# Optimization experiments

Measured on AMD Instinct MI355X. Metric: run time of the kernel, lower is better.

## Reference

```python
import jax, jax.numpy as jnp
import numpy as np

B, C, S, H, W = 1, 256, 64, 32, 128
BLOCKS, HEADS, DH = 2, 8, 32
SCALE = DH ** (-0.5)


def layer_norm(x, w, b, eps=1e-5):
    mu = jnp.mean(x, axis=-1, keepdims=True)
    var = jnp.var(x, axis=-1, keepdims=True)
    return (x - mu) * jax.lax.rsqrt(var + eps) * w + b


def generate_y_for_attn(y, u):
    # y: (B,C,H,W), u: (B,S,S) float -> (B, S^2, 2H, C)
    Bv, Cv, Hv, Wv = y.shape
    Sv = u.shape[1]
    uf = jnp.floor(u).reshape(Bv, Sv * Sv)
    u_left = jnp.clip(uf, 0, Wv - 1).astype(jnp.int32)
    u_right = jnp.clip(uf + 1, 0, Wv - 1).astype(jnp.int32)
    yf = y.reshape(Bv, Cv * Hv, Wv)

    def gather_w(idx):
        idxb = jnp.broadcast_to(idx[:, None, :], (Bv, Cv * Hv, Sv * Sv))
        return jnp.take_along_axis(yf, idxb, axis=2).reshape(Bv, Cv, Hv, Sv * Sv)

    ys = jnp.concatenate([gather_w(u_left), gather_w(u_right)], axis=2)  # (B,C,2H,S2)
    return ys.transpose(0, 3, 2, 1)  # (B, S2, 2H, C)


def cross_attention(x, y, p, i):
    # x: (B,M,C), y: (B,M,N,C)
    q = layer_norm(x, p['ln_q_w'][i], p['ln_q_b'][i]) @ p['Wq'][i]        # (B,M,HD)
    k = layer_norm(y, p['ln_k_w'][i], p['ln_k_b'][i]) @ p['Wk'][i]        # (B,M,N,HD)
    v = layer_norm(y, p['ln_v_w'][i], p['ln_v_b'][i]) @ p['Wv'][i]        # (B,M,N,HD)
    Bv, M, _ = q.shape
    N = k.shape[2]
    q = q.reshape(Bv, M, HEADS, DH)
    k = k.reshape(Bv, M, N, HEADS, DH)
    v = v.reshape(Bv, M, N, HEADS, DH)
    dot = SCALE * jnp.einsum('bmhd,bmnhd->bhmn', q, k)                    # (B,H,M,N)
    attn = jax.nn.softmax(dot, axis=-1)
    a = jnp.einsum('bhmn,bmnhd->bmhd', attn, v).reshape(Bv, M, HEADS * DH)
    z = a @ p['Wproj'][i] + p['bproj'][i]
    z = layer_norm(z, p['ln_pre_w'][i], p['ln_pre_b'][i])
    h = jax.nn.gelu(z @ p['Wm1'][i] + p['bm1'][i], approximate=False)
    z = z + (h @ p['Wm2'][i] + p['bm2'][i])
    return layer_norm(z, p['ln_post_w'][i], p['ln_post_b'][i])


def setup_inputs() -> dict:
    key = jax.random.key(0)
    ks = jax.random.split(key, 16)
    std = 0.02
    inp = {
        'grd2sat': jax.random.normal(ks[0], (B, C, S, S), jnp.float32),
        'grd_x': jax.random.normal(ks[1], (B, C, H, W), jnp.float32),
        'u': jax.random.uniform(ks[2], (B, S, S), jnp.float32) * (W - 1),
        'ln_q_w': jnp.ones((BLOCKS, C)), 'ln_q_b': jnp.zeros((BLOCKS, C)),
        'ln_k_w': jnp.ones((BLOCKS, C)), 'ln_k_b': jnp.zeros((BLOCKS, C)),
        'ln_v_w': jnp.ones((BLOCKS, C)), 'ln_v_b': jnp.zeros((BLOCKS, C)),
        'Wq': std * jax.random.normal(ks[3], (BLOCKS, C, HEADS * DH)),
        'Wk': std * jax.random.normal(ks[4], (BLOCKS, C, HEADS * DH)),
        'Wv': std * jax.random.normal(ks[5], (BLOCKS, C, HEADS * DH)),
        'Wproj': std * jax.random.normal(ks[6], (BLOCKS, HEADS * DH, C)),
        'bproj': jnp.zeros((BLOCKS, C)),
        'ln_pre_w': jnp.ones((BLOCKS, C)), 'ln_pre_b': jnp.zeros((BLOCKS, C)),
        'Wm1': std * jax.random.normal(ks[7], (BLOCKS, C, 2 * C)),
        'bm1': jnp.zeros((BLOCKS, 2 * C)),
        'Wm2': std * jax.random.normal(ks[8], (BLOCKS, 2 * C, C)),
        'bm2': jnp.zeros((BLOCKS, C)),
        'ln_post_w': jnp.ones((BLOCKS, C)), 'ln_post_b': jnp.zeros((BLOCKS, C)),
    }
    return inp


def reference(grd2sat, grd_x, u, ln_q_w, ln_q_b, ln_k_w, ln_k_b, ln_v_w, ln_v_b,
              Wq, Wk, Wv, Wproj, bproj, ln_pre_w, ln_pre_b, Wm1, bm1, Wm2, bm2,
              ln_post_w, ln_post_b):
    p = dict(ln_q_w=ln_q_w, ln_q_b=ln_q_b, ln_k_w=ln_k_w, ln_k_b=ln_k_b,
             ln_v_w=ln_v_w, ln_v_b=ln_v_b, Wq=Wq, Wk=Wk, Wv=Wv, Wproj=Wproj,
             bproj=bproj, ln_pre_w=ln_pre_w, ln_pre_b=ln_pre_b, Wm1=Wm1, bm1=bm1,
             Wm2=Wm2, bm2=bm2, ln_post_w=ln_post_w, ln_post_b=ln_post_b)
    y_attn = generate_y_for_attn(grd_x, u)               # (B, S^2, 2H, C)
    x = grd2sat.reshape(B, C, S * S).transpose(0, 2, 1)  # (B, M, C)
    for i in range(BLOCKS):
        # (Swin self-attention layer omitted; cross-attention stack only.)
        x = cross_attention(x, y_attn, p, i)
    out = x.transpose(0, 2, 1).reshape(B, C, S, S)
    # L2 normalize over channel dim
    norm = jnp.sqrt(jnp.sum(out * out, axis=1, keepdims=True))
    return out / jnp.maximum(norm, 1e-12)
```

## Files before the change

### kernel.cpp

```cpp
#include <hip/hip_runtime.h>
#include <math.h>


#define C_DIM 256
#define M_DIM 4096
#define W_DIM 128
#define H_DIM 32
#define ATT_SCALE 0.17677669529663687f

typedef __attribute__((ext_vector_type(8))) short short8;
typedef __attribute__((ext_vector_type(4))) short short4v;
typedef __attribute__((ext_vector_type(4))) float floatx4;

__device__ __forceinline__ unsigned short f2bf(float f) {
    unsigned u = __float_as_uint(f);
    unsigned r = (u + 0x7fffu + ((u >> 16) & 1u)) >> 16;
    return (unsigned short)r;
}
__device__ __forceinline__ float gelu_exact(float x) {
    return 0.5f * x * (1.0f + erff(x * 0.70710678118654752f));
}

struct PrepArgs {
    const float* grd2sat; float* xcur;
// ... 11 lines not shown
    int b = blockIdx.x, t = threadIdx.x;
    if (b < 256) {
        float (*tile)[65] = (float(*)[65])smemf;
        int m0 = (b & 63) << 6, c0 = (b >> 6) << 6;
        for (int it = 0; it < 16; ++it) {
            int idx = it * 256 + t;
            int co = idx >> 6, mo = idx & 63;
            tile[co][mo] = a.grd2sat[(size_t)(c0 + co) * M_DIM + m0 + mo];
        }
        __syncthreads();
        for (int it = 0; it < 16; ++it) {
            int idx = it * 256 + t;
            int mo = idx >> 6, co = idx & 63;
            a.xcur[(size_t)(m0 + mo) * C_DIM + c0 + co] = tile[co][mo];
        }
    } else if (b < 384) {
        int idx = b - 256;
        int h = idx & 31, w0 = (idx >> 5) << 5;
        float (*tile)[33] = (float(*)[33])smemf;
        float (*ps)[32] = (float(*)[32])(smemf + 8448);
        float (*pss)[32] = (float(*)[32])(smemf + 8704);
        float* mu_s = smemf + 8960;
        float* rs_s = smemf + 8992;
        int wo = t & 31, cb = t >> 5;
        for (int it = 0; it < 32; ++it) {
            int c = it * 8 + cb;
            tile[c][wo] = a.grd_x[(size_t)c * (H_DIM * W_DIM) + h * W_DIM + w0 + wo];
        }
        __syncthreads();
        {
            int w = t & 31, part = t >> 5;
            float s = 0.f, ss = 0.f;
            for (int c = part * 32; c < part * 32 + 32; ++c) {
                float x = tile[c][w];
                s += x; ss += x * x;
            }
            ps[part][w] = s; pss[part][w] = ss;
        }
        __syncthreads();
        if (t < 32) {
            float s = 0.f, ss = 0.f;
            for (int p = 0; p < 8; ++p) { s += ps[p][t]; ss += pss[p][t]; }
            float mu = s * (1.f / 256.f);
            float var = ss * (1.f / 256.f) - mu * mu;
            mu_s[t] = mu;
            rs_s[t] = rsqrtf(var + 1e-5f);
        }
        __syncthreads();
        for (int jj = 0; jj < 32; ++jj) {
            float mu = mu_s[jj], rs = rs_s[jj];
            a.yhat[((size_t)(w0 + jj) * H_DIM + h) * C_DIM + t] =
                (tile[t][jj] - mu) * rs;
        }
    } else if (b < 1408) {
        int wI = b - 384;
        int e = 0;
        while (wI >= a.wbase[e + 1]) ++e;
        int tl = wI - a.wbase[e];
        int tilesC = a.wC[e] >> 5;
        int tr = tl / tilesC, tc = tl - tr * tilesC;
        int r0 = tr << 5, c0 = tc << 5;
        const float* in = a.win[e];
        unsigned short* out = a.wout[e];
        const float* lnw = a.wlnw[e];
        int R = a.wR[e], Cc = a.wC[e];
        float (*tile)[33] = (float(*)[33])smemf;
        int rl = t >> 3, cq = (t & 7) << 2;
        float4 v = *(const float4*)&in[(size_t)(r0 + rl) * Cc + c0 + cq];
        if (lnw) {
            float s = lnw[r0 + rl];
            v.x *= s; v.y *= s; v.z *= s; v.w *= s;
        }
        tile[rl][cq + 0] = v.x;
        tile[rl][cq + 1] = v.y;
        tile[rl][cq + 2] = v.z;
        tile[rl][cq + 3] = v.w;
        __syncthreads();
        int cl = t >> 3, rq = (t & 7) << 2;
        ushort4 o;
        o.x = f2bf(tile[rq + 0][cl]);
        o.y = f2bf(tile[rq + 1][cl]);
        o.z = f2bf(tile[rq + 2][cl]);
        o.w = f2bf(tile[rq + 3][cl]);
        *(ushort4*)&out[(size_t)(c0 + cl) * R + r0 + rq] = o;
    } else if (b < 1418) {
        int jj = b - 1408;
        int N = a.fN[jj];
        int wcol = a.fwcol[jj] + t;
        const float* W = a.fW[jj];
        const float* lb = a.flnb[jj];
        float s = a.fbase[jj] ? a.fbase[jj][wcol] : 0.f;
        for (int k = 0; k < 256; ++k) s += lb[k] * W[(size_t)k * N + wcol];
        a.fout[jj][a.focol[jj] + t] = s;
    } else {
        int* hist = (int*)smemf;
        int* cur = (int*)smemf + 128;
        unsigned short* wlb = (unsigned short*)((int*)smemf + 256);
        if (t < 128) hist[t] = 0;
        __syncthreads();
        for (int it = 0; it < 16; ++it) {
            int m = it * 256 + t;
            int wl = (int)floorf(a.u[m]);
            wl = max(0, min(wl, 126));
            wlb[m] = (unsigned short)wl;
            atomicAdd(&hist[wl], 1);
        }
        __syncthreads();
        if (t == 0) {
            int run = 0, nc = 0;
            for (int bkt = 0; bkt < 127; ++bkt) {
                int c = hist[bkt];
                cur[bkt] = run;
                int q0 = run;
                while (c > 0) {
                    int take = min(c, 32);
                    a.chunks[nc] = make_int4(bkt, q0, take, 0);
                    ++nc; q0 += take; c -= take;
                }
                run += hist[bkt];
            }
            *a.nchunks = nc;
        }
        __syncthreads();
        for (int it = 0; it < 16; ++it) {
            int m = it * 256 + t;
            int wl = wlb[m];
            int pos = atomicAdd(&cur[wl], 1);
            a.perm[pos] = m;
        }
    }
}

struct GJ {
    const void* A; const unsigned short* Bt;
    const float* bias; const float* aw; const float* ab;
    const float* rw; const float* rb; const float* res;
    float* wrz; void* out; unsigned short* out2;
    int K, N;
};

template <int LN, int EPI, int OUTM, bool WRZ, bool ABF16>
__device__ __forceinline__ void gemm_core(const GJ& j, short (*As)[264],
                                          short (*Bs)[264], int bm, int by) {
    int t = threadIdx.x;
    int bn = by << 6;
    int wv = t >> 6, lane = t & 63;
    int mt = wv & 1, nt0 = (wv >> 1) << 1;
    int quad = lane >> 4, l16 = lane & 15;
    floatx4 acc0 = {0.f, 0.f, 0.f, 0.f};
    floatx4 acc1 = {0.f, 0.f, 0.f, 0.f};
    const int K = j.K;
    for (int kc = 0; kc < K; kc += 256) {
        if (kc) __syncthreads();
        if (ABF16) {
            int ar = t >> 3, cq = (t & 7) << 5;
            const unsigned short* ap =
                (const unsigned short*)j.A + (size_t)(bm + ar) * K + kc + cq;
#pragma unroll
            for (int c = 0; c < 4; ++c)
                *(uint4*)&As[ar][cq + (c << 3)] = *(const uint4*)(ap + (c << 3));
        } else {
            int ar = t >> 3, cq = (t & 7) << 2;
            const float* ap = (const float*)j.A + (size_t)(bm + ar) * K + kc + cq;
            float4 v[8];
#pragma unroll
            for (int g = 0; g < 8; ++g) v[g] = *(const float4*)(ap + g * 32);
            if (LN >= 1) {
                float s = 0.f, ss = 0.f;
#pragma unroll
                for (int g = 0; g < 8; ++g) {
                    s += v[g].x + v[g].y + v[g].z + v[g].w;
                    ss += v[g].x * v[g].x + v[g].y * v[g].y + v[g].z * v[g].z +
                          v[g].w * v[g].w;
                }
#pragma unroll
                for (int o = 1; o < 8; o <<= 1) {
                    s += __shfl_xor(s, o, 64);
                    ss += __shfl_xor(ss, o, 64);
                }
                float mu = s * (1.f / 256.f);
                float rs = rsqrtf(ss * (1.f / 256.f) - mu * mu + 1e-5f);
#pragma unroll
                for (int g = 0; g < 8; ++g) {
                    v[g].x = (v[g].x - mu) * rs;
                    v[g].y = (v[g].y - mu) * rs;
                    v[g].z = (v[g].z - mu) * rs;
                    v[g].w = (v[g].w - mu) * rs;
                }
            }
#pragma unroll
            for (int g = 0; g < 8; ++g) {
                short4v o;
                o[0] = (short)f2bf(v[g].x);
                o[1] = (short)f2bf(v[g].y);
                o[2] = (short)f2bf(v[g].z);
                o[3] = (short)f2bf(v[g].w);
                *(short4v*)&As[ar][cq + g * 32] = o;
            }
        }
        {
            int br = t >> 2, cq2 = (t & 3) << 3;
            const unsigned short* bp = j.Bt + (size_t)(bn + br) * K + kc + cq2;
#pragma unroll
            for (int g = 0; g < 8; ++g)
                *(short8*)&Bs[br][cq2 + g * 32] = *(const short8*)(bp + g * 32);
        }
        __syncthreads();
#pragma unroll
        for (int k0 = 0; k0 < 8; ++k0) {
            short8 aa = *(const short8*)&As[(mt << 4) + l16][(k0 << 5) + (quad << 3)];
            short8 b0 = *(const short8*)&Bs[(nt0 << 4) + l16][(k0 << 5) + (quad << 3)];
            short8 b1 =
                *(const short8*)&Bs[((nt0 + 1) << 4) + l16][(k0 << 5) + (quad << 3)];
            acc0 = __builtin_amdgcn_mfma_f32_16x16x32_bf16(aa, b0, acc0, 0, 0, 0);
            acc1 = __builtin_amdgcn_mfma_f32_16x16x32_bf16(aa, b1, acc1, 0, 0, 0);
        }
    }
#pragma unroll
    for (int jj = 0; jj < 2; ++jj) {
        const floatx4 accv = jj ? acc1 : acc0;
        int col = bn + ((nt0 + jj) << 4) + l16;
        float bv = j.bias ? j.bias[col] : 0.f;
#pragma unroll
        for (int r = 0; r < 4; ++r) {
            int row = bm + (mt << 4) + (quad << 2) + r;
            float v = accv[r] + bv;
            if (OUTM == 0) {
                ((float*)j.out)[(size_t)row * j.N + col] = v;
            } else if (OUTM == 1) {
                ((unsigned short*)j.out)[(size_t)row * j.N + col] = f2bf(v);
            } else {
                if (col < 256)
                    ((unsigned short*)j.out)[(size_t)row * 256 + col] = f2bf(v);
                else
                    j.out2[(size_t)(col - 256) * M_DIM + row] = f2bf(v);
            }
        }
    }
}

__global__ __launch_bounds__(256) void kv_kernel(GJ j0, GJ j1) {
    __shared__ short As[32][264];
    __shared__ short Bs[64][264];
    int bm = blockIdx.x << 5;
    if ((int)blockIdx.y < 8)
        gemm_core<0, 0, 2, false, false>(j0, As, Bs, bm, blockIdx.y);
    else
        gemm_core<0, 0, 2, false, false>(j1, As, Bs, bm, blockIdx.y - 8);
}

struct MegaArgs {
    const float* xcur;
    const int* perm; const int4* chunks; const int* nchunks;
    float* xfinal;
    const unsigned short* Wq[2]; const unsigned short* Wp[2];
    const unsigned short* Wm1[2]; const unsigned short* Wm2[2];
    const unsigned short* Ktb[2]; const unsigned short* Vtb[2];
    const float* qb[2]; const float* m1b[2];
    const float* bpj[2]; const float* bm2v[2];
    const float* pw[2]; const float* pb[2];
    const float* aw; const float* ab;
};

__device__ __forceinline__ void cg_pass(const short* As, int lda,
                                        const unsigned short* Bt, int K, int bn,
                                        short (*Bst)[264], floatx4& acc0,
                                        floatx4& acc1) {
    int t = threadIdx.x;
    int wv = t >> 6, lane = t & 63, quad = lane >> 4, l16 = lane & 15;
    int mt = wv & 1, nt0 = (wv >> 1) << 1;
    int br = t >> 2, cq2 = (t & 3) << 3;
#pragma unroll 1
    for (int kc = 0; kc < K; kc += 256) {
        const unsigned short* bp = Bt + (size_t)(bn + br) * K + kc + cq2;
#pragma unroll
        for (int g = 0; g < 8; ++g)
            *(short8*)&Bst[br][cq2 + (g << 5)] = *(const short8*)(bp + (g << 5));
        __syncthreads();
        const short* ap = As + (size_t)((mt << 4) + l16) * lda + kc + (quad << 3);
#pragma unroll
        for (int k0 = 0; k0 < 8; ++k0) {
            short8 aa = *(const short8*)(ap + (k0 << 5));
            short8 b0 =
                *(const short8*)&Bst[(nt0 << 4) + l16][(k0 << 5) + (quad << 3)];
            short8 b1 =
                *(const short8*)&Bst[((nt0 + 1) << 4) + l16][(k0 << 5) + (quad << 3)];
            acc0 = __builtin_amdgcn_mfma_f32_16x16x32_bf16(aa, b0, acc0, 0, 0, 0);
            acc1 = __builtin_amdgcn_mfma_f32_16x16x32_bf16(aa, b1, acc1, 0, 0, 0);
        }
        __syncthreads();
    }
}

__global__ __launch_bounds__(256) void mega_kernel(MegaArgs a) {
    __shared__ __align__(16) char smem[150656];
    short (*XH)[264] = (short(*)[264])(smem);
    short (*HH)[520] = (short(*)[520])(smem);
    short (*QR)[264] = (short(*)[264])(smem + 33280);
    float (*Zf)[260] = (float(*)[260])(smem + 33280);
    short (*ZH)[264] = (short(*)[264])(smem + 66560);
    short (*AR)[264] = (short(*)[264])(smem + 83456);
    float (*XO)[260] = (float(*)[260])(smem + 83456);
    short (*Bst)[264] = (short(*)[264])(smem + 116736);
    float (*SS)[69] = (float(*)[69])(smem + 116736);
    short (*PB)[72] = (short(*)[72])(smem + 116736 + 8832);
    int* gp = (int*)(smem + 150528);

    if ((int)blockIdx.x >= *a.nchunks) return;
    int4 cd = a.chunks[blockIdx.x];
    int wl = cd.x, qstart = cd.y, qcnt = cd.z;
    int t = threadIdx.x;
    if (t < 32) gp[t] = (t < qcnt) ? a.perm[qstart + t] : a.perm[qstart];
    __syncthreads();

    int wv = t >> 6, lane = t & 63, quad = lane >> 4, l16 = lane & 15;
    int mt = wv & 1, nt0 = (wv >> 1) << 1, ntP = wv >> 1;
    int r8 = t >> 3, cq = (t & 7) << 5;
    int sg = t & 7;

#pragma unroll 1
    for (int l = 0; l < 2; ++l) {
        {
            float4 v[8];
            if (l == 0) {
                const float* xp = a.xcur + (size_t)gp[r8] * 256 + cq;
#pragma unroll
                for (int g = 0; g < 8; ++g) v[g] = *(const float4*)(xp + (g << 2));
            } else {
#pragma unroll
                for (int g = 0; g < 8; ++g)
                    v[g] = *(const float4*)&XO[r8][cq + (g << 2)];
            }
            float s = 0.f, ss = 0.f;
#pragma unroll
            for (int g = 0; g < 8; ++g) {
                s += v[g].x + v[g].y + v[g].z + v[g].w;
                ss += v[g].x * v[g].x + v[g].y * v[g].y + v[g].z * v[g].z +
                      v[g].w * v[g].w;
            }
#pragma unroll
            for (int o = 1; o < 8; o <<= 1) {
                s += __shfl_xor(s, o, 64);
                ss += __shfl_xor(ss, o, 64);
            }
            float mu = s * (1.f / 256.f);
            float rs = rsqrtf(ss * (1.f / 256.f) - mu * mu + 1e-5f);
#pragma unroll
            for (int g = 0; g < 8; ++g) {
                v[g].x = (v[g].x - mu) * rs;
                v[g].y = (v[g].y - mu) * rs;
                v[g].z = (v[g].z - mu) * rs;
                v[g].w = (v[g].w - mu) * rs;
            }
            if (l == 1) {
                float s2 = 0.f, ss2 = 0.f;
#pragma unroll
                for (int g = 0; g < 8; ++g) {
                    float4 w4 = *(const float4*)&a.aw[cq + (g << 2)];
                    float4 b4 = *(const float4*)&a.ab[cq + (g << 2)];
                    v[g].x = v[g].x * w4.x + b4.x;
                    v[g].y = v[g].y * w4.y + b4.y;
                    v[g].z = v[g].z * w4.z + b4.z;
                    v[g].w = v[g].w * w4.w + b4.w;
                    s2 += v[g].x + v[g].y + v[g].z + v[g].w;
                    ss2 += v[g].x * v[g].x + v[g].y * v[g].y + v[g].z * v[g].z +
                           v[g].w * v[g].w;
                }
#pragma unroll
                for (int o = 1; o < 8; o <<= 1) {
                    s2 += __shfl_xor(s2, o, 64);
                    ss2 += __shfl_xor(ss2, o, 64);
                }
                float mu2 = s2 * (1.f / 256.f);
                float rs2 = rsqrtf(ss2 * (1.f / 256.f) - mu2 * mu2 + 1e-5f);
#pragma unroll
                for (int g = 0; g < 8; ++g) {
                    v[g].x = (v[g].x - mu2) * rs2;
                    v[g].y = (v[g].y - mu2) * rs2;
                    v[g].z = (v[g].z - mu2) * rs2;
                    v[g].w = (v[g].w - mu2) * rs2;
                }
            }
#pragma unroll
            for (int g = 0; g < 8; ++g) {
                short4v o;
                o[0] = (short)f2bf(v[g].x);
                o[1] = (short)f2bf(v[g].y);
                o[2] = (short)f2bf(v[g].z);
                o[3] = (short)f2bf(v[g].w);
                *(short4v*)&XH[r8][cq + (g << 2)] = o;
            }
        }
        __syncthreads();

        {
            const float* qb = a.qb[l];
#pragma unroll 1
            for (int bn = 0; bn < 256; bn += 64) {
                floatx4 a0 = {0.f, 0.f, 0.f, 0.f};
                floatx4 a1 = {0.f, 0.f, 0.f, 0.f};
                cg_pass((const short*)XH, 264, a.Wq[l], 256, bn, Bst, a0, a1);
#pragma unroll
                for (int jj = 0; jj < 2; ++jj) {
                    const floatx4 av = jj ? a1 : a0;
                    int col = bn + ((nt0 + jj) << 4) + l16;
                    float bv = qb[col];
#pragma unroll
                    for (int r = 0; r < 4; ++r)
                        QR[(mt << 4) + (quad << 2) + r][col] =
                            (short)f2bf(av[r] + bv);
                }
            }
        }
        __syncthreads();

        {
            const unsigned short* kp0 =
                a.Ktb[l] + ((size_t)((wl << 5) + (nt0 << 4) + l16)) * 256;
            const unsigned short* kp1 = kp0 + (16 * 256);
            const unsigned short* vpb =
                a.Vtb[l] + (size_t)((ntP << 4) + l16) * M_DIM + (wl << 5);
            short8 qa = *(const short8*)&QR[(mt << 4) + l16][(quad << 3)];
            short8 kb0 = *(const short8*)(kp0 + (quad << 3));
            short8 kb1 = *(const short8*)(kp1 + (quad << 3));
            short8 va0 = *(const short8*)(vpb + (quad << 3));
            short8 va1 = *(const short8*)(vpb + 32 + (quad << 3));
#pragma unroll 1
            for (int h = 0; h < 8; ++h) {
                {
                    floatx4 zz = {0.f, 0.f, 0.f, 0.f};
                    floatx4 c0 =
                        __builtin_amdgcn_mfma_f32_16x16x32_bf16(qa, kb0, zz, 0, 0, 0);
                    floatx4 c1 =
                        __builtin_amdgcn_mfma_f32_16x16x32_bf16(qa, kb1, zz, 0, 0, 0);
#pragma unroll
                    for (int r = 0; r < 4; ++r) {
                        int row = (mt << 4) + (quad << 2) + r;
                        SS[row][(nt0 << 4) + l16] = c0[r];
                        SS[row][((nt0 + 1) << 4) + l16] = c1[r];
                    }
                }
                short8 nva0 = va0, nva1 = va1;
                if (h < 7) {
                    int hn = h + 1;
                    qa = *(const short8*)&QR[(mt << 4) + l16][(hn << 5) + (quad << 3)];
                    kb0 = *(const short8*)(kp0 + (hn << 5) + (quad << 3));
                    kb1 = *(const short8*)(kp1 + (hn << 5) + (quad << 3));
                    const unsigned short* vpn = vpb + (size_t)(hn << 5) * M_DIM;
                    nva0 = *(const short8*)(vpn + (quad << 3));
                    nva1 = *(const short8*)(vpn + 32 + (quad << 3));
                }
                __syncthreads();
                {
                    float e[8];
                    float s = 0.f;
#pragma unroll
                    for (int c = 0; c < 8; ++c) {
                        e[c] = __expf(SS[r8][(sg << 3) + c] * ATT_SCALE);
                        s += e[c];
                    }
                    s += __shfl_xor(s, 1, 64);
                    s += __shfl_xor(s, 2, 64);
                    s += __shfl_xor(s, 4, 64);
                    float ri = 1.f / s;
#pragma unroll
                    for (int c = 0; c < 8; ++c)
                        PB[r8][(sg << 3) + c] = (short)f2bf(e[c] * ri);
                }
                __syncthreads();
                {
                    floatx4 acc = {0.f, 0.f, 0.f, 0.f};
#pragma unroll
                    for (int ks = 0; ks < 2; ++ks) {
                        short8 pa = *(const short8*)&PB[(mt << 4) + l16]
                                                      [(ks << 5) + (quad << 3)];
                        short8 vb = ks ? va1 : va0;
                        acc = __builtin_amdgcn_mfma_f32_16x16x32_bf16(pa, vb, acc,
                                                                      0, 0, 0);
                    }
#pragma unroll
                    for (int r = 0; r < 4; ++r)
                        AR[(mt << 4) + (quad << 2) + r]
                          [(h << 5) + (ntP << 4) + l16] = (short)f2bf(acc[r]);
                }
                va0 = nva0;
                va1 = nva1;
            }
        }
        __syncthreads();

        {
            const float* bpj = a.bpj[l];
#pragma unroll 1
            for (int bn = 0; bn < 256; bn += 64) {
                floatx4 a0 = {0.f, 0.f, 0.f, 0.f};
                floatx4 a1 = {0.f, 0.f, 0.f, 0.f};
                cg_pass((const short*)AR, 264, a.Wp[l], 256, bn, Bst, a0, a1);
#pragma unroll
                for (int jj = 0; jj < 2; ++jj) {
                    const floatx4 av = jj ? a1 : a0;
                    int col = bn + ((nt0 + jj) << 4) + l16;
                    float bv = bpj[col];
#pragma unroll
                    for (int r = 0; r < 4; ++r)
                        Zf[(mt << 4) + (quad << 2) + r][col] = av[r] + bv;
                }
            }
        }
        __syncthreads();

        {
            const float* pw = a.pw[l];
            const float* pb = a.pb[l];
            float4 v[8];
#pragma unroll
            for (int g = 0; g < 8; ++g) v[g] = *(const float4*)&Zf[r8][cq + (g << 2)];
            float s = 0.f, ss = 0.f;
#pragma unroll
            for (int g = 0; g < 8; ++g) {
                s += v[g].x + v[g].y + v[g].z + v[g].w;
                ss += v[g].x * v[g].x + v[g].y * v[g].y + v[g].z * v[g].z +
                      v[g].w * v[g].w;
            }
#pragma unroll
            for (int o = 1; o < 8; o <<= 1) {
                s += __shfl_xor(s, o, 64);
                ss += __shfl_xor(ss, o, 64);
            }
            float mu = s * (1.f / 256.f);
            float rs = rsqrtf(ss * (1.f / 256.f) - mu * mu + 1e-5f);
#pragma unroll
            for (int g = 0; g < 8; ++g) {
                float4 z;
                z.x = (v[g].x - mu) * rs;
                z.y = (v[g].y - mu) * rs;
                z.z = (v[g].z - mu) * rs;
                z.w = (v[g].w - mu) * rs;
                short4v o;
                o[0] = (short)f2bf(z.x);
                o[1] = (short)f2bf(z.y);
                o[2] = (short)f2bf(z.z);
                o[3] = (short)f2bf(z.w);
                *(short4v*)&ZH[r8][cq + (g << 2)] = o;
                float4 w4 = *(const float4*)&pw[cq + (g << 2)];
                float4 b4 = *(const float4*)&pb[cq + (g << 2)];
                float4 za;
                za.x = z.x * w4.x + b4.x;
                za.y = z.y * w4.y + b4.y;
                za.z = z.z * w4.z + b4.z;
                za.w = z.w * w4.w + b4.w;
                *(float4*)&Zf[r8][cq + (g << 2)] = za;
            }
        }
        __syncthreads();

        {
            const float* m1b = a.m1b[l];
#pragma unroll 1
            for (int bn = 0; bn < 512; bn += 64) {
                floatx4 a0 = {0.f, 0.f, 0.f, 0.f};
                floatx4 a1 = {0.f, 0.f, 0.f, 0.f};
                cg_pass((const short*)ZH, 264, a.Wm1[l], 256, bn, Bst, a0, a1);
#pragma unroll
                for (int jj = 0; jj < 2; ++jj) {
                    const floatx4 av = jj ? a1 : a0;
                    int col = bn + ((nt0 + jj) << 4) + l16;
                    float bv = m1b[col];
#pragma unroll
                    for (int r = 0; r < 4; ++r)
                        HH[(mt << 4) + (quad << 2) + r][col] =
                            (short)f2bf(gelu_exact(av[r] + bv));
                }
            }
        }
        __syncthreads();

        {
            const float* b2 = a.bm2v[l];
#pragma unroll 1
            for (int bn = 0; bn < 256; bn += 64) {
                floatx4 a0 = {0.f, 0.f, 0.f, 0.f};
                floatx4 a1 = {0.f, 0.f, 0.f, 0.f};
                cg_pass((const short*)HH, 520, a.Wm2[l], 512, bn, Bst, a0, a1);
#pragma unroll
                for (int jj = 0; jj < 2; ++jj) {
                    const floatx4 av = jj ? a1 : a0;
                    int col = bn + ((nt0 + jj) << 4) + l16;
                    float bv = b2[col];
#pragma unroll
                    for (int r = 0; r < 4; ++r) {
                        int row = (mt << 4) + (quad << 2) + r;
                        float v = av[r] + bv + Zf[row][col];
                        if (l == 0) {
                            XO[row][col] = v;
                        } else if (row < qcnt) {
                            a.xfinal[(size_t)gp[row] * 256 + col] = v;
                        }
                    }
                }
            }
        }
        __syncthreads();
    }
}

__global__ __launch_bounds__(256) void out_kernel(const float* __restrict__ X,
                                                  const float* __restrict__ w,
                                                  const float* __restrict__ b,
                                                  float* __restrict__ out) {
    __shared__ float tile[64][65];
    int t = threadIdx.x;
    int mo = t >> 2, q = t & 3;
    int m0 = blockIdx.x << 6;
    const float* p = X + (size_t)(m0 + mo) * C_DIM + (q << 6);
    float4 v[16];
    float s = 0.f, ss = 0.f;
#pragma unroll
    for (int c = 0; c < 16; ++c) {
        v[c] = *(const float4*)(p + c * 4);
        s += v[c].x + v[c].y + v[c].z + v[c].w;
        ss += v[c].x * v[c].x + v[c].y * v[c].y + v[c].z * v[c].z + v[c].w * v[c].w;
    }
    s += __shfl_xor(s, 1, 64); s += __shfl_xor(s, 2, 64);
    ss += __shfl_xor(ss, 1, 64); ss += __shfl_xor(ss, 2, 64);
    float mu = s * (1.f / 256.f);
    float rs = rsqrtf(ss * (1.f / 256.f) - mu * mu + 1e-5f);
    float ss2 = 0.f;
#pragma unroll
    for (int c = 0; c < 16; ++c) {
        float4 w4 = *(const float4*)&w[(q << 6) + c * 4];
        float4 b4 = *(const float4*)&b[(q << 6) + c * 4];
        v[c].x = (v[c].x - mu) * rs * w4.x + b4.x;
        v[c].y = (v[c].y - mu) * rs * w4.y + b4.y;
        v[c].z = (v[c].z - mu) * rs * w4.z + b4.z;
        v[c].w = (v[c].w - mu) * rs * w4.w + b4.w;
        ss2 += v[c].x * v[c].x + v[c].y * v[c].y + v[c].z * v[c].z + v[c].w * v[c].w;
    }
    ss2 += __shfl_xor(ss2, 1, 64); ss2 += __shfl_xor(ss2, 2, 64);
    float sc = 1.f / fmaxf(sqrtf(ss2), 1e-12f);
    for (int cc = 0; cc < 4; ++cc) {
        if (q == cc) {
#pragma unroll
            for (int c = 0; c < 16; ++c) {
                tile[mo][c * 4 + 0] = v[c].x * sc;
                tile[mo][c * 4 + 1] = v[c].y * sc;
                tile[mo][c * 4 + 2] = v[c].z * sc;
                tile[mo][c * 4 + 3] = v[c].w * sc;
            }
        }
        __syncthreads();
        for (int it = 0; it < 16; ++it) {
            int idx = it * 256 + t;
            int co = idx >> 6, mr = idx & 63;
            out[(size_t)((cc << 6) + co) * M_DIM + m0 + mr] = tile[mr][co];
        }
        __syncthreads();
    }
}

extern "C" void kernel_launch(void* const* d_in, const int* in_sizes, int n_in,
                              void* d_out, int out_size, void* d_ws, size_t ws_size,
                              hipStream_t stream) {
    const float* grd2sat = (const float*)d_in[0];
    const float* grd_x   = (const float*)d_in[1];
    const float* u       = (const float*)d_in[2];
    const float* ln_q_w  = (const float*)d_in[3];
    const float* ln_q_b  = (const float*)d_in[4];
    const float* ln_k_w  = (const float*)d_in[5];
    const float* ln_k_b  = (const float*)d_in[6];
    const float* ln_v_w  = (const float*)d_in[7];
    const float* ln_v_b  = (const float*)d_in[8];
    const float* Wq      = (const float*)d_in[9];
    const float* Wk      = (const float*)d_in[10];
    const float* Wv      = (const float*)d_in[11];
    const float* Wproj   = (const float*)d_in[12];
    const float* bproj   = (const float*)d_in[13];
    const float* ln_pre_w = (const float*)d_in[14];
    const float* ln_pre_b = (const float*)d_in[15];
    const float* Wm1     = (const float*)d_in[16];
    const float* bm1     = (const float*)d_in[17];
    const float* Wm2     = (const float*)d_in[18];
    const float* bm2     = (const float*)d_in[19];
    const float* ln_post_w = (const float*)d_in[20];
    const float* ln_post_b = (const float*)d_in[21];

    float* ws   = (float*)d_ws;
    float* yhat = ws;
    float* xcur = ws + 1048576;
    float* zq   = ws + 2097152;
    unsigned short* Ktab0 = (unsigned short*)(ws + 6291456);
    unsigned short* Vt0   = (unsigned short*)(ws + 6815744);
    unsigned short* Ktab1 = (unsigned short*)(ws + 7340032);
    unsigned short* Vt1   = (unsigned short*)(ws + 7864320);
    unsigned short* Bt    = (unsigned short*)(ws + 8388608);
    float* biasbuf = ws + 8912896;
    int*  perm    = (int*)(ws + 8915456);
    int4* chunks  = (int4*)(ws + 8919552);
    int*  nchunks = (int*)(ws + 8921600);
    const size_t BS = 524288;
    const size_t OQ = 0, OKV = 65536, OP = 196608, OM1 = 262144, OM2 = 393216;

    dim3 b256(256);

    PrepArgs pa;
    pa.grd2sat = grd2sat; pa.xcur = xcur;
    pa.grd_x = grd_x;     pa.yhat = yhat;
    pa.u = u; pa.perm = perm; pa.chunks = chunks; pa.nchunks = nchunks;
    {
        int base = 0;
        for (int i = 0; i < 2; ++i) {
            int e = 6 * i;
            unsigned short* bt = Bt + i * BS;
            pa.win[e+0] = Wq + i * 65536;    pa.wout[e+0] = bt + OQ;
            pa.wlnw[e+0] = ln_q_w + i * 256; pa.wR[e+0] = 256; pa.wC[e+0] = 256;
            pa.win[e+1] = Wk + i * 65536;    pa.wout[e+1] = bt + OKV;
            pa.wlnw[e+1] = ln_k_w + i * 256; pa.wR[e+1] = 256; pa.wC[e+1] = 256;
            pa.win[e+2] = Wv + i * 65536;    pa.wout[e+2] = bt + OKV + 65536;
            pa.wlnw[e+2] = ln_v_w + i * 256; pa.wR[e+2] = 256; pa.wC[e+2] = 256;
            pa.win[e+3] = Wproj + i * 65536; pa.wout[e+3] = bt + OP;
            pa.wlnw[e+3] = nullptr;          pa.wR[e+3] = 256; pa.wC[e+3] = 256;
            pa.win[e+4] = Wm1 + i * 131072;  pa.wout[e+4] = bt + OM1;
            pa.wlnw[e+4] = ln_pre_w + i * 256; pa.wR[e+4] = 256; pa.wC[e+4] = 512;
            pa.win[e+5] = Wm2 + i * 131072;  pa.wout[e+5] = bt + OM2;
            pa.wlnw[e+5] = nullptr;          pa.wR[e+5] = 512; pa.wC[e+5] = 256;
        }
        for (int e = 0; e < 12; ++e) {
            pa.wbase[e] = base;
            base += (pa.wR[e] >> 5) * (pa.wC[e] >> 5);
        }
        pa.wbase[12] = base;
        for (int i = 0; i < 2; ++i) {
            int jb = 5 * i;
            float* bb = biasbuf + i * 1280;
            pa.fW[jb+0] = Wq + i * 65536; pa.flnb[jb+0] = ln_q_b + i * 256;
            pa.fbase[jb+0] = nullptr; pa.fout[jb+0] = bb;
            pa.fN[jb+0] = 256; pa.fwcol[jb+0] = 0; pa.focol[jb+0] = 0;
            pa.fW[jb+1] = Wk + i * 65536; pa.flnb[jb+1] = ln_k_b + i * 256;
            pa.fbase[jb+1] = nullptr; pa.fout[jb+1] = bb + 256;
            pa.fN[jb+1] = 256; pa.fwcol[jb+1] = 0; pa.focol[jb+1] = 0;
            pa.fW[jb+2] = Wv + i * 65536; pa.flnb[jb+2] = ln_v_b + i * 256;
            pa.fbase[jb+2] = nullptr; pa.fout[jb+2] = bb + 256;
            pa.fN[jb+2] = 256; pa.fwcol[jb+2] = 0; pa.focol[jb+2] = 256;
            pa.fW[jb+3] = Wm1 + i * 131072; pa.flnb[jb+3] = ln_pre_b + i * 256;
            pa.fbase[jb+3] = bm1 + i * 512; pa.fout[jb+3] = bb + 768;
            pa.fN[jb+3] = 512; pa.fwcol[jb+3] = 0; pa.focol[jb+3] = 0;
            pa.fW[jb+4] = Wm1 + i * 131072; pa.flnb[jb+4] = ln_pre_b + i * 256;
            pa.fbase[jb+4] = bm1 + i * 512; pa.fout[jb+4] = bb + 768;
            pa.fN[jb+4] = 512; pa.fwcol[jb+4] = 256; pa.focol[jb+4] = 256;
        }
    }
// ... 32 lines not shown
```

Before: 238.4 us.

## Read weights directly from global in mega kernel GEMMs with 8-tile register accumulators

Replaces the LDS-staged B-tile GEMM passes (cg_pass, with two syncs per 64-column chunk) with mgemm8, which loads weight fragments straight from global/L2 into registers and has each wave accumulate 8 output tiles (128 columns). The attention stage is restructured to process heads in pairs, with separate score, softmax and PV phases and per-pair score/probability buffers. The MLP is split into two 256-wide halves so the hidden buffer fits in reused LDS. Shared memory drops and launch bounds are set to one block, trading LDS staging and barriers for more global load traffic and higher register pressure. Unused template branches in the KV GEMM are also removed.

```diff
diff --git a/kernel.cpp b/kernel.cpp
--- a/kernel.cpp
+++ b/kernel.cpp
@@ -187,42 +187,12 @@
     const int K = j.K;
     for (int kc = 0; kc < K; kc += 256) {
         if (kc) __syncthreads();
-        if (ABF16) {
-            int ar = t >> 3, cq = (t & 7) << 5;
-            const unsigned short* ap =
-                (const unsigned short*)j.A + (size_t)(bm + ar) * K + kc + cq;
-#pragma unroll
-            for (int c = 0; c < 4; ++c)
-                *(uint4*)&As[ar][cq + (c << 3)] = *(const uint4*)(ap + (c << 3));
-        } else {
+        {
             int ar = t >> 3, cq = (t & 7) << 2;
             const float* ap = (const float*)j.A + (size_t)(bm + ar) * K + kc + cq;
             float4 v[8];
 #pragma unroll
             for (int g = 0; g < 8; ++g) v[g] = *(const float4*)(ap + g * 32);
-            if (LN >= 1) {
-                float s = 0.f, ss = 0.f;
-#pragma unroll
-                for (int g = 0; g < 8; ++g) {
-                    s += v[g].x + v[g].y + v[g].z + v[g].w;
-                    ss += v[g].x * v[g].x + v[g].y * v[g].y + v[g].z * v[g].z +
-                          v[g].w * v[g].w;
-                }
-#pragma unroll
-                for (int o = 1; o < 8; o <<= 1) {
-                    s += __shfl_xor(s, o, 64);
-                    ss += __shfl_xor(ss, o, 64);
-                }
-                float mu = s * (1.f / 256.f);
-                float rs = rsqrtf(ss * (1.f / 256.f) - mu * mu + 1e-5f);
-#pragma unroll
-                for (int g = 0; g < 8; ++g) {
-                    v[g].x = (v[g].x - mu) * rs;
-                    v[g].y = (v[g].y - mu) * rs;
-                    v[g].z = (v[g].z - mu) * rs;
-                    v[g].w = (v[g].w - mu) * rs;
-                }
-            }
 #pragma unroll
             for (int g = 0; g < 8; ++g) {
                 short4v o;
@@ -260,16 +230,10 @@
         for (int r = 0; r < 4; ++r) {
             int row = bm + (mt << 4) + (quad << 2) + r;
             float v = accv[r] + bv;
-            if (OUTM == 0) {
-                ((float*)j.out)[(size_t)row * j.N + col] = v;
-            } else if (OUTM == 1) {
-                ((unsigned short*)j.out)[(size_t)row * j.N + col] = f2bf(v);
-            } else {
-                if (col < 256)
-                    ((unsigned short*)j.out)[(size_t)row * 256 + col] = f2bf(v);
-                else
-                    j.out2[(size_t)(col - 256) * M_DIM + row] = f2bf(v);
-            }
+            if (col < 256)
+                ((unsigned short*)j.out)[(size_t)row * 256 + col] = f2bf(v);
+            else
+                j.out2[(size_t)(col - 256) * M_DIM + row] = f2bf(v);
         }
     }
 }
@@ -297,49 +261,35 @@
     const float* aw; const float* ab;
 };
 
-__device__ __forceinline__ void cg_pass(const short* As, int lda,
-                                        const unsigned short* Bt, int K, int bn,
-                                        short (*Bst)[264], floatx4& acc0,
-                                        floatx4& acc1) {
-    int t = threadIdx.x;
-    int wv = t >> 6, lane = t & 63, quad = lane >> 4, l16 = lane & 15;
-    int mt = wv & 1, nt0 = (wv >> 1) << 1;
-    int br = t >> 2, cq2 = (t & 3) << 3;
-#pragma unroll 1
-    for (int kc = 0; kc < K; kc += 256) {
-        const unsigned short* bp = Bt + (size_t)(bn + br) * K + kc + cq2;
-#pragma unroll
-        for (int g = 0; g < 8; ++g)
-            *(short8*)&Bst[br][cq2 + (g << 5)] = *(const short8*)(bp + (g << 5));
-        __syncthreads();
-        const short* ap = As + (size_t)((mt << 4) + l16) * lda + kc + (quad << 3);
-#pragma unroll
-        for (int k0 = 0; k0 < 8; ++k0) {
-            short8 aa = *(const short8*)(ap + (k0 << 5));
-            short8 b0 =
-                *(const short8*)&Bst[(nt0 << 4) + l16][(k0 << 5) + (quad << 3)];
-            short8 b1 =
-                *(const short8*)&Bst[((nt0 + 1) << 4) + l16][(k0 << 5) + (quad << 3)];
-            acc0 = __builtin_amdgcn_mfma_f32_16x16x32_bf16(aa, b0, acc0, 0, 0, 0);
-            acc1 = __builtin_amdgcn_mfma_f32_16x16x32_bf16(aa, b1, acc1, 0, 0, 0);
-        }
-        __syncthreads();
-    }
-}
-
-__global__ __launch_bounds__(256) void mega_kernel(MegaArgs a) {
-    __shared__ __align__(16) char smem[150656];
+__device__ __forceinline__ void mgemm8(const short* As, int lda,
+                                       const unsigned short* Bt, int Kstride,
+                                       int kcB, int laneRow, int colbase,
+                                       int quad, int l16, floatx4 acc[8]) {
+    const short* ap = As + (size_t)laneRow * lda + (quad << 3);
+    const unsigned short* bp =
+        Bt + (size_t)(colbase + l16) * Kstride + kcB + (quad << 3);
+#pragma unroll
+    for (int k0 = 0; k0 < 8; ++k0) {
+        short8 aa = *(const short8*)(ap + (k0 << 5));
+#pragma unroll
+        for (int i = 0; i < 8; ++i) {
+            short8 bb =
+                *(const short8*)(bp + (size_t)(i << 4) * Kstride + (k0 << 5));
+            acc[i] = __builtin_amdgcn_mfma_f32_16x16x32_bf16(aa, bb, acc[i], 0, 0, 0);
+        }
+    }
+}
+
+__global__ __launch_bounds__(256, 1) void mega_kernel(MegaArgs a) {
+    __shared__ __align__(16) char smem[127616];
     short (*XH)[264] = (short(*)[264])(smem);
-    short (*HH)[520] = (short(*)[520])(smem);
-    short (*QR)[264] = (short(*)[264])(smem + 33280);
-    float (*Zf)[260] = (float(*)[260])(smem + 33280);
-    short (*ZH)[264] = (short(*)[264])(smem + 66560);
-    short (*AR)[264] = (short(*)[264])(smem + 83456);
-    float (*XO)[260] = (float(*)[260])(smem + 83456);
-    short (*Bst)[264] = (short(*)[264])(smem + 116736);
-    float (*SS)[69] = (float(*)[69])(smem + 116736);
-    short (*PB)[72] = (short(*)[72])(smem + 116736 + 8832);
-    int* gp = (int*)(smem + 150528);
+    short (*QR)[264] = (short(*)[264])(smem + 16896);
+    short (*ZH)[264] = (short(*)[264])(smem + 33792);
+    short (*AR)[264] = (short(*)[264])(smem + 50688);
+    float (*Zf)[260] = (float(*)[260])(smem + 67584);
+    float (*SS)[32][68] = (float(*)[32][68])(smem + 100864);
+    short (*PB)[32][72] = (short(*)[32][72])(smem + 118272);
+    int* gp = (int*)(smem + 127488);
 
     if ((int)blockIdx.x >= *a.nchunks) return;
     int4 cd = a.chunks[blockIdx.x];
@@ -349,29 +299,30 @@
     __syncthreads();
 
     int wv = t >> 6, lane = t & 63, quad = lane >> 4, l16 = lane & 15;
-    int mt = wv & 1, nt0 = (wv >> 1) << 1, ntP = wv >> 1;
+    int mt = wv & 1, g = wv >> 1;
+    int laneRow = (mt << 4) + l16;
+    int colbase = g << 7;
     int r8 = t >> 3, cq = (t & 7) << 5;
-    int sg = t & 7;
-
-#pragma unroll 1
+
+#pragma unroll
     for (int l = 0; l < 2; ++l) {
         {
             float4 v[8];
             if (l == 0) {
                 const float* xp = a.xcur + (size_t)gp[r8] * 256 + cq;
 #pragma unroll
-                for (int g = 0; g < 8; ++g) v[g] = *(const float4*)(xp + (g << 2));
+                for (int gg = 0; gg < 8; ++gg) v[gg] = *(const float4*)(xp + (gg << 2));
             } else {
 #pragma unroll
-                for (int g = 0; g < 8; ++g)
-                    v[g] = *(const float4*)&XO[r8][cq + (g << 2)];
+                for (int gg = 0; gg < 8; ++gg)
+                    v[gg] = *(const float4*)&Zf[r8][cq + (gg << 2)];
             }
             float s = 0.f, ss = 0.f;
 #pragma unroll
-            for (int g = 0; g < 8; ++g) {
-                s += v[g].x + v[g].y + v[g].z + v[g].w;
-                ss += v[g].x * v[g].x + v[g].y * v[g].y + v[g].z * v[g].z +
-                      v[g].w * v[g].w;
+            for (int gg = 0; gg < 8; ++gg) {
+                s += v[gg].x + v[gg].y + v[gg].z + v[gg].w;
+                ss += v[gg].x * v[gg].x + v[gg].y * v[gg].y + v[gg].z * v[gg].z +
+                      v[gg].w * v[gg].w;
             }
 #pragma unroll
             for (int o = 1; o < 8; o <<= 1) {
@@ -381,25 +332,25 @@
             float mu = s * (1.f / 256.f);
             float rs = rsqrtf(ss * (1.f / 256.f) - mu * mu + 1e-5f);
 #pragma unroll
-            for (int g = 0; g < 8; ++g) {
-                v[g].x = (v[g].x - mu) * rs;
-                v[g].y = (v[g].y - mu) * rs;
-                v[g].z = (v[g].z - mu) * rs;
-                v[g].w = (v[g].w - mu) * rs;
+            for (int gg = 0; gg < 8; ++gg) {
+                v[gg].x = (v[gg].x - mu) * rs;
+                v[gg].y = (v[gg].y - mu) * rs;
+                v[gg].z = (v[gg].z - mu) * rs;
+                v[gg].w = (v[gg].w - mu) * rs;
             }
             if (l == 1) {
                 float s2 = 0.f, ss2 = 0.f;
 #pragma unroll
-                for (int g = 0; g < 8; ++g) {
-                    float4 w4 = *(const float4*)&a.aw[cq + (g << 2)];
-                    float4 b4 = *(const float4*)&a.ab[cq + (g << 2)];
-                    v[g].x = v[g].x * w4.x + b4.x;
-                    v[g].y = v[g].y * w4.y + b4.y;
-                    v[g].z = v[g].z * w4.z + b4.z;
-                    v[g].w = v[g].w * w4.w + b4.w;
-                    s2 += v[g].x + v[g].y + v[g].z + v[g].w;
-                    ss2 += v[g].x * v[g].x + v[g].y * v[g].y + v[g].z * v[g].z +
-                           v[g].w * v[g].w;
+                for (int gg = 0; gg < 8; ++gg) {
+                    float4 w4 = *(const float4*)&a.aw[cq + (gg << 2)];
+                    float4 b4 = *(const float4*)&a.ab[cq + (gg << 2)];
+                    v[gg].x = v[gg].x * w4.x + b4.x;
+                    v[gg].y = v[gg].y * w4.y + b4.y;
+                    v[gg].z = v[gg].z * w4.z + b4.z;
+                    v[gg].w = v[gg].w * w4.w + b4.w;
+                    s2 += v[gg].x + v[gg].y + v[gg].z + v[gg].w;
+                    ss2 += v[gg].x * v[gg].x + v[gg].y * v[gg].y + v[gg].z * v[gg].z +
+                           v[gg].w * v[gg].w;
                 }
 #pragma unroll
                 for (int o = 1; o < 8; o <<= 1) {
@@ -409,137 +360,142 @@
                 float mu2 = s2 * (1.f / 256.f);
                 float rs2 = rsqrtf(ss2 * (1.f / 256.f) - mu2 * mu2 + 1e-5f);
 #pragma unroll
-                for (int g = 0; g < 8; ++g) {
-                    v[g].x = (v[g].x - mu2) * rs2;
-                    v[g].y = (v[g].y - mu2) * rs2;
-                    v[g].z = (v[g].z - mu2) * rs2;
-                    v[g].w = (v[g].w - mu2) * rs2;
-                }
-            }
-#pragma unroll
-            for (int g = 0; g < 8; ++g) {
+                for (int gg = 0; gg < 8; ++gg) {
+                    v[gg].x = (v[gg].x - mu2) * rs2;
+                    v[gg].y = (v[gg].y - mu2) * rs2;
+                    v[gg].z = (v[gg].z - mu2) * rs2;
+                    v[gg].w = (v[gg].w - mu2) * rs2;
+                }
+            }
+#pragma unroll
+            for (int gg = 0; gg < 8; ++gg) {
                 short4v o;
-                o[0] = (short)f2bf(v[g].x);
-                o[1] = (short)f2bf(v[g].y);
-                o[2] = (short)f2bf(v[g].z);
-                o[3] = (short)f2bf(v[g].w);
-                *(short4v*)&XH[r8][cq + (g << 2)] = o;
-            }
-        }
-        __syncthreads();
-
-        {
+                o[0] = (short)f2bf(v[gg].x);
+                o[1] = (short)f2bf(v[gg].y);
+                o[2] = (short)f2bf(v[gg].z);
+                o[3] = (short)f2bf(v[gg].w);
+                *(short4v*)&XH[r8][cq + (gg << 2)] = o;
+            }
+        }
+        __syncthreads();
+
+        {
+            floatx4 acc[8];
+#pragma unroll
+            for (int i = 0; i < 8; ++i) acc[i] = (floatx4){0.f, 0.f, 0.f, 0.f};
+            mgemm8((const short*)XH, 264, a.Wq[l], 256, 0, laneRow, colbase,
+                   quad, l16, acc);
             const float* qb = a.qb[l];
+#pragma unroll
+            for (int i = 0; i < 8; ++i) {
+                int col = colbase + (i << 4) + l16;
+                float bv = qb[col];
+#pragma unroll
+                for (int r = 0; r < 4; ++r)
+                    QR[(mt << 4) + (quad << 2) + r][col] = (short)f2bf(acc[i][r] + bv);
+            }
+        }
+        __syncthreads();
+
+        {
+            const unsigned short* Ktb = a.Ktb[l];
+            const unsigned short* Vtb = a.Vtb[l];
+            int p = g;
+            int mtA = mt;
+            auto scores = [&](int hd) {
+                short8 qa =
+                    *(const short8*)&QR[(mtA << 4) + l16][(hd << 5) + (quad << 3)];
+                const unsigned short* kbase =
+                    Ktb + (size_t)(wl << 5) * 256 + (hd << 5) + (quad << 3);
+                floatx4 c[4];
+#pragma unroll
+                for (int ct = 0; ct < 4; ++ct) {
+                    short8 kb =
+                        *(const short8*)(kbase + (size_t)((ct << 4) + l16) * 256);
+                    floatx4 z = {0.f, 0.f, 0.f, 0.f};
+                    c[ct] = __builtin_amdgcn_mfma_f32_16x16x32_bf16(qa, kb, z, 0, 0, 0);
+                }
+#pragma unroll
+                for (int ct = 0; ct < 4; ++ct)
+#pragma unroll
+                    for (int r = 0; r < 4; ++r)
+                        SS[p][(mtA << 4) + (quad << 2) + r][(ct << 4) + l16] =
+                            c[ct][r];
+            };
+            auto pv = [&](int hd) {
+                floatx4 o0 = {0.f, 0.f, 0.f, 0.f}, o1 = {0.f, 0.f, 0.f, 0.f};
+                const unsigned short* vb = Vtb +
+                    (size_t)((hd << 5) + l16) * M_DIM + (wl << 5) + (quad << 3);
+#pragma unroll
+                for (int ks = 0; ks < 2; ++ks) {
+                    short8 pa = *(const short8*)&PB[p][(mtA << 4) + l16]
+                                                  [(ks << 5) + (quad << 3)];
+                    short8 v0 = *(const short8*)(vb + (ks << 5));
+                    short8 v1 =
+                        *(const short8*)(vb + (size_t)16 * M_DIM + (ks << 5));
+                    o0 = __builtin_amdgcn_mfma_f32_16x16x32_bf16(pa, v0, o0, 0, 0, 0);
+                    o1 = __builtin_amdgcn_mfma_f32_16x16x32_bf16(pa, v1, o1, 0, 0, 0);
+                }
+#pragma unroll
+                for (int r = 0; r < 4; ++r) {
+                    int row = (mtA << 4) + (quad << 2) + r;
+                    AR[row][(hd << 5) + l16] = (short)f2bf(o0[r]);
+                    AR[row][(hd << 5) + 16 + l16] = (short)f2bf(o1[r]);
+                }
+            };
+            auto softmax = [&]() {
+                int p2 = t >> 7;
+                int row2 = (t >> 2) & 31;
+                int sg2 = t & 3;
+                float e[16];
+                float s = 0.f;
+#pragma unroll
+                for (int c = 0; c < 16; ++c) {
+                    e[c] = __expf(SS[p2][row2][(sg2 << 4) + c] * ATT_SCALE);
+                    s += e[c];
+                }
+                s += __shfl_xor(s, 1, 64);
+                s += __shfl_xor(s, 2, 64);
+                float ri = 1.f / s;
+                short8 o0, o1;
+#pragma unroll
+                for (int c = 0; c < 8; ++c) o0[c] = (short)f2bf(e[c] * ri);
+#pragma unroll
+                for (int c = 0; c < 8; ++c) o1[c] = (short)f2bf(e[c + 8] * ri);
+                *(short8*)&PB[p2][row2][(sg2 << 4)] = o0;
+                *(short8*)&PB[p2][row2][(sg2 << 4) + 8] = o1;
+            };
+
+            scores(p);
+            __syncthreads();
+            softmax();
+            __syncthreads();
 #pragma unroll 1
-            for (int bn = 0; bn < 256; bn += 64) {
-                floatx4 a0 = {0.f, 0.f, 0.f, 0.f};
-                floatx4 a1 = {0.f, 0.f, 0.f, 0.f};
-                cg_pass((const short*)XH, 264, a.Wq[l], 256, bn, Bst, a0, a1);
-#pragma unroll
-                for (int jj = 0; jj < 2; ++jj) {
-                    const floatx4 av = jj ? a1 : a0;
-                    int col = bn + ((nt0 + jj) << 4) + l16;
-                    float bv = qb[col];
-#pragma unroll
-                    for (int r = 0; r < 4; ++r)
-                        QR[(mt << 4) + (quad << 2) + r][col] =
-                            (short)f2bf(av[r] + bv);
-                }
-            }
-        }
-        __syncthreads();
-
-        {
-            const unsigned short* kp0 =
-                a.Ktb[l] + ((size_t)((wl << 5) + (nt0 << 4) + l16)) * 256;
-            const unsigned short* kp1 = kp0 + (16 * 256);
-            const unsigned short* vpb =
-                a.Vtb[l] + (size_t)((ntP << 4) + l16) * M_DIM + (wl << 5);
-            short8 qa = *(const short8*)&QR[(mt << 4) + l16][(quad << 3)];
-            short8 kb0 = *(const short8*)(kp0 + (quad << 3));
-            short8 kb1 = *(const short8*)(kp1 + (quad << 3));
-            short8 va0 = *(const short8*)(vpb + (quad << 3));
-            short8 va1 = *(const short8*)(vpb + 32 + (quad << 3));
-#pragma unroll 1
-            for (int h = 0; h < 8; ++h) {
-                {
-                    floatx4 zz = {0.f, 0.f, 0.f, 0.f};
-                    floatx4 c0 =
-                        __builtin_amdgcn_mfma_f32_16x16x32_bf16(qa, kb0, zz, 0, 0, 0);
-                    floatx4 c1 =
-                        __builtin_amdgcn_mfma_f32_16x16x32_bf16(qa, kb1, zz, 0, 0, 0);
-#pragma unroll
-                    for (int r = 0; r < 4; ++r) {
-                        int row = (mt << 4) + (quad << 2) + r;
-                        SS[row][(nt0 << 4) + l16] = c0[r];
-                        SS[row][((nt0 + 1) << 4) + l16] = c1[r];
-                    }
-                }
-                short8 nva0 = va0, nva1 = va1;
-                if (h < 7) {
-                    int hn = h + 1;
-                    qa = *(const short8*)&QR[(mt << 4) + l16][(hn << 5) + (quad << 3)];
-                    kb0 = *(const short8*)(kp0 + (hn << 5) + (quad << 3));
-                    kb1 = *(const short8*)(kp1 + (hn << 5) + (quad << 3));
-                    const unsigned short* vpn = vpb + (size_t)(hn << 5) * M_DIM;
-                    nva0 = *(const short8*)(vpn + (quad << 3));
-                    nva1 = *(const short8*)(vpn + 32 + (quad << 3));
-                }
+            for (int it = 0; it < 4; ++it) {
+                pv((it << 1) + p);
+                if (it < 3) scores(((it + 1) << 1) + p);
                 __syncthreads();
-                {
-                    float e[8];
-                    float s = 0.f;
-#pragma unroll
-                    for (int c = 0; c < 8; ++c) {
-                        e[c] = __expf(SS[r8][(sg << 3) + c] * ATT_SCALE);
-                        s += e[c];
-                    }
-                    s += __shfl_xor(s, 1, 64);
-                    s += __shfl_xor(s, 2, 64);
-                    s += __shfl_xor(s, 4, 64);
-                    float ri = 1.f / s;
-#pragma unroll
-                    for (int c = 0; c < 8; ++c)
-                        PB[r8][(sg << 3) + c] = (short)f2bf(e[c] * ri);
-                }
-                __syncthreads();
-                {
-                    floatx4 acc = {0.f, 0.f, 0.f, 0.f};
-#pragma unroll
-                    for (int ks = 0; ks < 2; ++ks) {
-                        short8 pa = *(const short8*)&PB[(mt << 4) + l16]
-                                                      [(ks << 5) + (quad << 3)];
-                        short8 vb = ks ? va1 : va0;
-                        acc = __builtin_amdgcn_mfma_f32_16x16x32_bf16(pa, vb, acc,
-                                                                      0, 0, 0);
-                    }
-#pragma unroll
-                    for (int r = 0; r < 4; ++r)
-                        AR[(mt << 4) + (quad << 2) + r]
-                          [(h << 5) + (ntP << 4) + l16] = (short)f2bf(acc[r]);
-                }
-                va0 = nva0;
-                va1 = nva1;
-            }
-        }
-        __syncthreads();
-
-        {
+                if (it < 3) {
+                    softmax();
+                    __syncthreads();
+                }
+            }
+        }
+
+        {
+            floatx4 acc[8];
+#pragma unroll
+            for (int i = 0; i < 8; ++i) acc[i] = (floatx4){0.f, 0.f, 0.f, 0.f};
+            mgemm8((const short*)AR, 264, a.Wp[l], 256, 0, laneRow, colbase,
+                   quad, l16, acc);
             const float* bpj = a.bpj[l];
-#pragma unroll 1
-            for (int bn = 0; bn < 256; bn += 64) {
-                floatx4 a0 = {0.f, 0.f, 0.f, 0.f};
-                floatx4 a1 = {0.f, 0.f, 0.f, 0.f};
-                cg_pass((const short*)AR, 264, a.Wp[l], 256, bn, Bst, a0, a1);
-#pragma unroll
-                for (int jj = 0; jj < 2; ++jj) {
-                    const floatx4 av = jj ? a1 : a0;
-                    int col = bn + ((nt0 + jj) << 4) + l16;
-                    float bv = bpj[col];
-#pragma unroll
-                    for (int r = 0; r < 4; ++r)
-                        Zf[(mt << 4) + (quad << 2) + r][col] = av[r] + bv;
-                }
+#pragma unroll
+            for (int i = 0; i < 8; ++i) {
+                int col = colbase + (i << 4) + l16;
+                float bv = bpj[col];
+#pragma unroll
+                for (int r = 0; r < 4; ++r)
+                    Zf[(mt << 4) + (quad << 2) + r][col] = acc[i][r] + bv;
             }
         }
         __syncthreads();
@@ -549,13 +505,14 @@
             const float* pb = a.pb[l];
             float4 v[8];
 #pragma unroll
-            for (int g = 0; g < 8; ++g) v[g] = *(const float4*)&Zf[r8][cq + (g << 2)];
+            for (int gg = 0; gg < 8; ++gg)
+                v[gg] = *(const float4*)&Zf[r8][cq + (gg << 2)];
             float s = 0.f, ss = 0.f;
 #pragma unroll
-            for (int g = 0; g < 8; ++g) {
-                s += v[g].x + v[g].y + v[g].z + v[g].w;
-                ss += v[g].x * v[g].x + v[g].y * v[g].y + v[g].z * v[g].z +
-                      v[g].w * v[g].w;
+            for (int gg = 0; gg < 8; ++gg) {
+                s += v[gg].x + v[gg].y + v[gg].z + v[gg].w;
+                ss += v[gg].x * v[gg].x + v[gg].y * v[gg].y + v[gg].z * v[gg].z +
+                      v[gg].w * v[gg].w;
             }
 #pragma unroll
             for (int o = 1; o < 8; o <<= 1) {
@@ -565,72 +522,91 @@
             float mu = s * (1.f / 256.f);
             float rs = rsqrtf(ss * (1.f / 256.f) - mu * mu + 1e-5f);
 #pragma unroll
-            for (int g = 0; g < 8; ++g) {
+            for (int gg = 0; gg < 8; ++gg) {
                 float4 z;
-                z.x = (v[g].x - mu) * rs;
-                z.y = (v[g].y - mu) * rs;
-                z.z = (v[g].z - mu) * rs;
-                z.w = (v[g].w - mu) * rs;
+                z.x = (v[gg].x - mu) * rs;
+                z.y = (v[gg].y - mu) * rs;
+                z.z = (v[gg].z - mu) * rs;
+                z.w = (v[gg].w - mu) * rs;
                 short4v o;
                 o[0] = (short)f2bf(z.x);
                 o[1] = (short)f2bf(z.y);
                 o[2] = (short)f2bf(z.z);
                 o[3] = (short)f2bf(z.w);
-                *(short4v*)&ZH[r8][cq + (g << 2)] = o;
-                float4 w4 = *(const float4*)&pw[cq + (g << 2)];
-                float4 b4 = *(const float4*)&pb[cq + (g << 2)];
+                *(short4v*)&ZH[r8][cq + (gg << 2)] = o;
+                float4 w4 = *(const float4*)&pw[cq + (gg << 2)];
+                float4 b4 = *(const float4*)&pb[cq + (gg << 2)];
                 float4 za;
                 za.x = z.x * w4.x + b4.x;
                 za.y = z.y * w4.y + b4.y;
                 za.z = z.z * w4.z + b4.z;
                 za.w = z.w * w4.w + b4.w;
-                *(float4*)&Zf[r8][cq + (g << 2)] = za;
-            }
-        }
-        __syncthreads();
-
-        {
-            const float* m1b = a.m1b[l];
-#pragma unroll 1
-            for (int bn = 0; bn < 512; bn += 64) {
-                floatx4 a0 = {0.f, 0.f, 0.f, 0.f};
-                floatx4 a1 = {0.f, 0.f, 0.f, 0.f};
-                cg_pass((const short*)ZH, 264, a.Wm1[l], 256, bn, Bst, a0, a1);
-#pragma unroll
-                for (int jj = 0; jj < 2; ++jj) {
-                    const floatx4 av = jj ? a1 : a0;
-                    int col = bn + ((nt0 + jj) << 4) + l16;
-                    float bv = m1b[col];
-#pragma unroll
-                    for (int r = 0; r < 4; ++r)
-                        HH[(mt << 4) + (quad << 2) + r][col] =
-                            (short)f2bf(gelu_exact(av[r] + bv));
-                }
-            }
-        }
-        __syncthreads();
-
-        {
+                *(float4*)&Zf[r8][cq + (gg << 2)] = za;
+            }
+        }
+        __syncthreads();
+
+        short (*HH0)[264] = XH;
+        short (*HH1)[264] = QR;
+        const float* m1b = a.m1b[l];
+        {
+            floatx4 acc[8];
+#pragma unroll
+            for (int i = 0; i < 8; ++i) acc[i] = (floatx4){0.f, 0.f, 0.f, 0.f};
+            mgemm8((const short*)ZH, 264, a.Wm1[l], 256, 0, laneRow, colbase,
+                   quad, l16, acc);
+#pragma unroll
+            for (int i = 0; i < 8; ++i) {
+                int col = colbase + (i << 4) + l16;
+                float bv = m1b[col];
+#pragma unroll
+                for (int r = 0; r < 4; ++r)
+                    HH0[(mt << 4) + (quad << 2) + r][col] =
+                        (short)f2bf(gelu_exact(acc[i][r] + bv));
+            }
+        }
+        __syncthreads();
+
+        floatx4 macc[8];
+#pragma unroll
+        for (int i = 0; i < 8; ++i) macc[i] = (floatx4){0.f, 0.f, 0.f, 0.f};
+
+        {
+            floatx4 acc[8];
+#pragma unroll
+            for (int i = 0; i < 8; ++i) acc[i] = (floatx4){0.f, 0.f, 0.f, 0.f};
+            mgemm8((const short*)ZH, 264, a.Wm1[l] + (size_t)256 * 256, 256, 0,
+                   laneRow, colbase, quad, l16, acc);
+            mgemm8((const short*)HH0, 264, a.Wm2[l], 512, 0, laneRow, colbase,
+                   quad, l16, macc);
+#pragma unroll
+            for (int i = 0; i < 8; ++i) {
+                int col = colbase + (i << 4) + l16;
+                float bv = m1b[256 + col];
+#pragma unroll
+                for (int r = 0; r < 4; ++r)
+                    HH1[(mt << 4) + (quad << 2) + r][col] =
+                        (short)f2bf(gelu_exact(acc[i][r] + bv));
+            }
+        }
+        __syncthreads();
+
+        {
+            mgemm8((const short*)HH1, 264, a.Wm2[l], 512, 256, laneRow, colbase,
+                   quad, l16, macc);
             const float* b2 = a.bm2v[l];
-#pragma unroll 1
-            for (int bn = 0; bn < 256; bn += 64) {
-                floatx4 a0 = {0.f, 0.f, 0.f, 0.f};
-                floatx4 a1 = {0.f, 0.f, 0.f, 0.f};
-                cg_pass((const short*)HH, 520, a.Wm2[l], 512, bn, Bst, a0, a1);
-#pragma unroll
-                for (int jj = 0; jj < 2; ++jj) {
-                    const floatx4 av = jj ? a1 : a0;
-                    int col = bn + ((nt0 + jj) << 4) + l16;
-                    float bv = b2[col];
-#pragma unroll
-                    for (int r = 0; r < 4; ++r) {
-                        int row = (mt << 4) + (quad << 2) + r;
-                        float v = av[r] + bv + Zf[row][col];
-                        if (l == 0) {
-                            XO[row][col] = v;
-                        } else if (row < qcnt) {
-                            a.xfinal[(size_t)gp[row] * 256 + col] = v;
-                        }
+#pragma unroll
+            for (int i = 0; i < 8; ++i) {
+                int col = colbase + (i << 4) + l16;
+                float bv = b2[col];
+#pragma unroll
+                for (int r = 0; r < 4; ++r) {
+                    int row = (mt << 4) + (quad << 2) + r;
+                    float v = macc[i][r] + bv + Zf[row][col];
+                    if (l == 0) {
+                        Zf[row][col] = v;
+                    } else if (row < qcnt) {
+                        a.xfinal[(size_t)gp[row] * 256 + col] = v;
                     }
                 }
             }
```

Result: slower. 287.9 us (+20.8%).
